# Performance work log

Measured on AMD Instinct MI355X. Metric: run time of the kernel, lower is better.

Reference implementation:

```python
import jax, jax.numpy as jnp
import numpy as np

MAX_LEN = 128
VOCAB = 32000
SENTINEL = 2**30  # larger than any valid token id; pushes masked slots to the end after sort


def setup_inputs() -> dict:
    key = jax.random.key(0)
    k1, k2, k3, k4 = jax.random.split(key, 4)
    B, L = 262144, MAX_LEN
    input_ids = jax.random.randint(k1, (B, L), 0, VOCAB, dtype=jnp.int32)
    attention_mask = jax.random.randint(k2, (B, L), 0, 2, dtype=jnp.int32)
    # MLP params: Linear(3,32) -> ReLU -> Linear(32,32) -> ReLU
    W1 = jax.random.normal(k3, (3, 32), dtype=jnp.float32) * (1.0 / np.sqrt(3.0))
    b1 = jnp.zeros((32,), dtype=jnp.float32)
    W2 = jax.random.normal(k4, (32, 32), dtype=jnp.float32) * (1.0 / np.sqrt(32.0))
    b2 = jnp.zeros((32,), dtype=jnp.float32)
    return {"input_ids": input_ids, "attention_mask": attention_mask,
            "W1": W1, "b1": b1, "W2": W2, "b2": b2}


def _symbolic_feats(input_ids, attention_mask):
    # Batched replacement of the per-row torch.unique loop:
    # sort masked tokens per row, count boundaries between distinct values.
    mask = attention_mask.astype(bool)
    seq_len = jnp.sum(mask, axis=1)  # [B]
    ids_m = jnp.where(mask, input_ids, SENTINEL)  # masked-out slots -> sentinel
    s = jnp.sort(ids_m, axis=1)  # valid tokens first (ids < SENTINEL)
    valid = s < SENTINEL
    first = jnp.ones((s.shape[0], 1), dtype=bool)
    new_val = jnp.concatenate([first, s[:, 1:] != s[:, :-1]], axis=1)
    uniq = jnp.sum(valid & new_val, axis=1)  # [B] unique count among valid tokens
    seq_f = seq_len.astype(jnp.float32)
    uniq_f = uniq.astype(jnp.float32)
    uniq_ratio = jnp.where(seq_len > 0, uniq_f / jnp.maximum(seq_f, 1.0), 0.0)
    feats = jnp.stack([seq_f / MAX_LEN, uniq_f / MAX_LEN, uniq_ratio], axis=1)  # [B,3]
    return feats


def reference(input_ids, attention_mask, W1, b1, W2, b2):
    feats = _symbolic_feats(input_ids, attention_mask)  # [B,3]
    h = jax.nn.relu(feats @ W1 + b1)
    out = jax.nn.relu(h @ W2 + b2)
    return out
```

## Files before the change

### kernel.cpp

```cpp
#include <hip/hip_runtime.h>

#define ROW_LEN 128
#define NPAIR (129 * 129)

__global__ __launch_bounds__(256) void mlp_table_kernel(
    const float* __restrict__ W1, const float* __restrict__ b1,
    const float* __restrict__ W2, const float* __restrict__ b2,
    float* __restrict__ table)
{
    const int tid = blockIdx.x * 256 + threadIdx.x;
    if (tid >= NPAIR * 32) return;
    const int p = tid >> 5;
    const int j = tid & 31;
    const int seq  = p / 129;
    const int uniq = p % 129;
    const float f0 = (float)seq  * (1.0f / 128.0f);
    const float f1 = (float)uniq * (1.0f / 128.0f);
    const float f2 = (seq > 0) ? ((float)uniq / (float)seq) : 0.0f;

    float acc = b2[j];
    #pragma unroll
    for (int jj = 0; jj < 32; ++jj) {
        float h = b1[jj];
        h = fmaf(f0, W1[jj],      h);
        h = fmaf(f1, W1[32 + jj], h);
        h = fmaf(f2, W1[64 + jj], h);
        h = fmaxf(h, 0.0f);
        acc = fmaf(h, W2[jj * 32 + j], acc);
    }
    table[tid] = fmaxf(acc, 0.0f);
}

__global__ __launch_bounds__(256) void rows_kernel(
    const int* __restrict__ ids, const int* __restrict__ amask,
    const float* __restrict__ table, float* __restrict__ out, int B)
{
    __shared__ unsigned bm[4][1024];

    const int wave = threadIdx.x >> 6;
    const int lane = threadIdx.x & 63;
    const int row  = blockIdx.x * 4 + wave;
    if (row >= B) return;

    uint4* mybm4 = (uint4*)bm[wave];
    #pragma unroll
    for (int i = 0; i < 4; ++i) mybm4[lane + i * 64] = make_uint4(0u, 0u, 0u, 0u);

    const long vbase = (long)row * (ROW_LEN / 2) + lane;
    const int2 id2 = ((const int2*)ids)[vbase];
    const int2 mk2 = ((const int2*)amask)[vbase];

    unsigned* mybm = bm[wave];
    int sl = 0, cnt = 0;
    if (mk2.x != 0) {
        sl++;
        const unsigned tok = (unsigned)id2.x;
        const unsigned m = 1u << (tok & 31u);
        const unsigned old = atomicOr(&mybm[tok >> 5], m);
        cnt += ((old & m) == 0u);
    }
    if (mk2.y != 0) {
        sl++;
        const unsigned tok = (unsigned)id2.y;
        const unsigned m = 1u << (tok & 31u);
        const unsigned old = atomicOr(&mybm[tok >> 5], m);
        cnt += ((old & m) == 0u);
    }

    unsigned packed = (unsigned)sl | ((unsigned)cnt << 16);
    #pragma unroll
    for (int off = 1; off < 64; off <<= 1)
        packed += __shfl_xor(packed, off, 64);

    const int seq  = (int)(packed & 0xFFFFu);
    const int uniq = (int)(packed >> 16);

    if (lane < 32) {
        const int p = seq * 129 + uniq;
        out[(long)row * 32 + lane] = table[p * 32 + lane];
    }
}

extern "C" void kernel_launch(void* const* d_in, const int* in_sizes, int n_in,
                              void* d_out, int out_size, void* d_ws, size_t ws_size,
                              hipStream_t stream) {
    const int*   ids   = (const int*)d_in[0];
    const int*   amask = (const int*)d_in[1];
    const float* W1    = (const float*)d_in[2];
    const float* b1    = (const float*)d_in[3];
    const float* W2    = (const float*)d_in[4];
    const float* b2    = (const float*)d_in[5];
    float* out   = (float*)d_out;
    float* table = (float*)d_ws;

    const int B = in_sizes[0] / ROW_LEN;

    const int tblThreads = NPAIR * 32;
    mlp_table_kernel<<<(tblThreads + 255) / 256, 256, 0, stream>>>(W1, b1, W2, b2, table);

    rows_kernel<<<(B + 3) / 4, 256, 0, stream>>>(ids, amask, table, out, B);
}
```

Measured before the change: 292.1 us.

## Process two rows per wave with int4 loads and ballot-popcount reductions

```diff
diff --git a/kernel.cpp b/kernel.cpp
--- a/kernel.cpp
+++ b/kernel.cpp
@@ -35,50 +35,59 @@
     const int* __restrict__ ids, const int* __restrict__ amask,
     const float* __restrict__ table, float* __restrict__ out, int B)
 {
-    __shared__ unsigned bm[4][1024];
+    __shared__ unsigned bm[8][1024];
 
     const int wave = threadIdx.x >> 6;
     const int lane = threadIdx.x & 63;
-    const int row  = blockIdx.x * 4 + wave;
-    if (row >= B) return;
+    const int half = lane >> 5;
+    const long pair = (long)blockIdx.x * 4 + wave;
+    if (pair * 2 >= B) return;
 
-    uint4* mybm4 = (uint4*)bm[wave];
+    const long v = pair * 64 + lane;
+    const int4 id4 = ((const int4*)ids)[v];
+    const int4 mk4 = ((const int4*)amask)[v];
+
+    uint4* z = (uint4*)bm[wave * 2];
     #pragma unroll
-    for (int i = 0; i < 4; ++i) mybm4[lane + i * 64] = make_uint4(0u, 0u, 0u, 0u);
+    for (int i = 0; i < 8; ++i) z[lane + i * 64] = make_uint4(0u, 0u, 0u, 0u);
 
-    const long vbase = (long)row * (ROW_LEN / 2) + lane;
-    const int2 id2 = ((const int2*)ids)[vbase];
-    const int2 mk2 = ((const int2*)amask)[vbase];
+    unsigned* mybm = bm[wave * 2 + half];
 
-    unsigned* mybm = bm[wave];
-    int sl = 0, cnt = 0;
-    if (mk2.x != 0) {
-        sl++;
-        const unsigned tok = (unsigned)id2.x;
-        const unsigned m = 1u << (tok & 31u);
-        const unsigned old = atomicOr(&mybm[tok >> 5], m);
-        cnt += ((old & m) == 0u);
+    int n0 = 0, n1 = 0, n2 = 0, n3 = 0;
+    if (mk4.x != 0) {
+        const unsigned t = (unsigned)id4.x, m = 1u << (t & 31u);
+        n0 = ((atomicOr(&mybm[t >> 5], m) & m) == 0u);
     }
-    if (mk2.y != 0) {
-        sl++;
-        const unsigned tok = (unsigned)id2.y;
-        const unsigned m = 1u << (tok & 31u);
-        const unsigned old = atomicOr(&mybm[tok >> 5], m);
-        cnt += ((old & m) == 0u);
+    if (mk4.y != 0) {
+        const unsigned t = (unsigned)id4.y, m = 1u << (t & 31u);
+        n1 = ((atomicOr(&mybm[t >> 5], m) & m) == 0u);
+    }
+    if (mk4.z != 0) {
+        const unsigned t = (unsigned)id4.z, m = 1u << (t & 31u);
+        n2 = ((atomicOr(&mybm[t >> 5], m) & m) == 0u);
+    }
+    if (mk4.w != 0) {
+        const unsigned t = (unsigned)id4.w, m = 1u << (t & 31u);
+        n3 = ((atomicOr(&mybm[t >> 5], m) & m) == 0u);
     }
 
-    unsigned packed = (unsigned)sl | ((unsigned)cnt << 16);
-    #pragma unroll
-    for (int off = 1; off < 64; off <<= 1)
-        packed += __shfl_xor(packed, off, 64);
+    const unsigned long long s0 = __ballot(mk4.x != 0);
+    const unsigned long long s1 = __ballot(mk4.y != 0);
+    const unsigned long long s2 = __ballot(mk4.z != 0);
+    const unsigned long long s3 = __ballot(mk4.w != 0);
+    const unsigned long long u0 = __ballot(n0 != 0);
+    const unsigned long long u1 = __ballot(n1 != 0);
+    const unsigned long long u2 = __ballot(n2 != 0);
+    const unsigned long long u3 = __ballot(n3 != 0);
 
-    const int seq  = (int)(packed & 0xFFFFu);
-    const int uniq = (int)(packed >> 16);
+    const int sh = lane & 32;
+    const int seq  = __popc((unsigned)(s0 >> sh)) + __popc((unsigned)(s1 >> sh))
+                   + __popc((unsigned)(s2 >> sh)) + __popc((unsigned)(s3 >> sh));
+    const int uniq = __popc((unsigned)(u0 >> sh)) + __popc((unsigned)(u1 >> sh))
+                   + __popc((unsigned)(u2 >> sh)) + __popc((unsigned)(u3 >> sh));
 
-    if (lane < 32) {
-        const int p = seq * 129 + uniq;
-        out[(long)row * 32 + lane] = table[p * 32 + lane];
-    }
+    const int p = seq * 129 + uniq;
+    out[pair * 64 + lane] = table[p * 32 + (lane & 31)];
 }
 
 extern "C" void kernel_launch(void* const* d_in, const int* in_sizes, int n_in,
@@ -98,5 +107,5 @@
     const int tblThreads = NPAIR * 32;
     mlp_table_kernel<<<(tblThreads + 255) / 256, 256, 0, stream>>>(W1, b1, W2, b2, table);
 
-    rows_kernel<<<(B + 3) / 4, 256, 0, stream>>>(ids, amask, table, out, B);
+    rows_kernel<<<(B + 7) / 8, 256, 0, stream>>>(ids, amask, table, out, B);
 }
```

New measurement: 281.1 us. 3.8% less time.
